# Performance work log

Measured on AMD Instinct MI355X. Metric: run time of the kernel, lower is better.

## Reference

```python
import jax, jax.numpy as jnp
import numpy as np


def setup_inputs() -> dict:
    key = jax.random.key(0)
    k1, k2, k3 = jax.random.split(key, 3)
    B, T, F, U = 32, 4096, 512, 512
    x = jax.random.normal(k1, (B, T, F), dtype=jnp.float32)
    W = jax.random.normal(k2, (F, U), dtype=jnp.float32)
    b = jnp.zeros((U,), dtype=jnp.float32)
    V = jax.random.uniform(k3, (U, 1), dtype=jnp.float32)
    return {"x": x, "W": W, "b": b, "V": V}


def reference(x, W, b, V):
    # u = tanh(x @ W + b): [B, T, U]
    u = jnp.tanh(jnp.einsum('btf,fu->btu', x, W) + b)
    # scores = u @ V: [B, T, 1]; softmax over time (dim=1)
    a = jax.nn.softmax(jnp.einsum('btu,uo->bto', u, V), axis=1)
    # weighted sum pooling over time -> [B, F]
    return jnp.sum(x * a, axis=1)
```

## Files before the change

### kernel.cpp

```cpp
#include <hip/hip_runtime.h>


#define XT 4096
#define XF 512
#define XU 512

typedef __attribute__((ext_vector_type(8))) short short8;
typedef __attribute__((ext_vector_type(16))) float f32x16;

__device__ inline void cvt_hilo(float x, unsigned short &h, unsigned short &l) {
  unsigned u = __builtin_bit_cast(unsigned, x);
  h = (unsigned short)(u >> 16);
  float hf = __builtin_bit_cast(float, u & 0xFFFF0000u);
  float lo = x - hf;
  l = (unsigned short)(__builtin_bit_cast(unsigned, lo) >> 16);
}

__device__ inline float tanh_fast(float z) {
  float e = __expf(2.0f * z);
  return 1.0f - 2.0f * __builtin_amdgcn_rcpf(e + 1.0f);
}

__global__ void wconv_kernel(const float *__restrict__ W,
                             unsigned short *__restrict__ whi,
                             unsigned short *__restrict__ wlo) {
  int t2 = blockIdx.x * 256 + threadIdx.x;
  int l = t2 & 31;
  int g = (t2 >> 5) & 1;
  int t = (t2 >> 6) & 15;
  int s = t2 >> 10;
  short8 hv, lv;
#pragma unroll
  for (int j = 0; j < 8; ++j) {
    unsigned short h, lo;
    cvt_hilo(W[(size_t)(s * 16 + g * 8 + j) * XU + t * 32 + l], h, lo);
    hv[j] = (short)h;
    lv[j] = (short)lo;
  }
  size_t off = (size_t)s * 8192 + t * 512 + g * 256 + l * 8;
  *(short8 *)(whi + off) = hv;
  *(short8 *)(wlo + off) = lv;
}

#define MFMA(a, b, c) __builtin_amdgcn_mfma_f32_32x32x16_bf16(a, b, c, 0, 0, 0)

__global__ __launch_bounds__(512, 2)
void gemm_scores_kernel(const float *__restrict__ x,
                        const unsigned short *__restrict__ whi,
                        const unsigned short *__restrict__ wlo,
                        const float *__restrict__ bias,
                        const float *__restrict__ V,
                        float *__restrict__ partial,
                        float *__restrict__ pstats) {
  __shared__ float scb[512];
  __shared__ float warr[128];
  __shared__ float red[1536];

  const int tid = threadIdx.x;
  const int lane = tid & 63;
  const int wave = tid >> 6;
  const int wr = wave >> 2;
  const int wc = wave & 3;
  const int l31 = lane & 31;
  const int half = lane >> 5;
  const size_t rowbase = (size_t)blockIdx.x * 128;

  f32x16 acc[2][4];
#pragma unroll
  for (int a = 0; a < 2; ++a)
#pragma unroll
    for (int c = 0; c < 4; ++c)
#pragma unroll
      for (int r = 0; r < 16; ++r) acc[a][c][r] = 0.f;

  const float *xr0 = x + (rowbase + wr * 64 + l31) * XF + half * 8;
  const float *xr1 = xr0 + 32 * XF;
  const unsigned short *whp = whi + (size_t)(wc * 4) * 512 + lane * 8;
  const unsigned short *wlp = wlo + (size_t)(wc * 4) * 512 + lane * 8;

#pragma unroll 1
  for (int s = 0; s < 32; ++s) {
    short8 bh[4], bl[4];
    const unsigned short *p = whp + (size_t)s * 8192;
    const unsigned short *q = wlp + (size_t)s * 8192;
#pragma unroll
    for (int cf = 0; cf < 4; ++cf) {
      bh[cf] = *(const short8 *)(p + cf * 512);
      bl[cf] = *(const short8 *)(q + cf * 512);
    }
    float4 a00 = *(const float4 *)(xr0 + s * 16);
    float4 a01 = *(const float4 *)(xr0 + s * 16 + 4);
    float4 a10 = *(const float4 *)(xr1 + s * 16);
    float4 a11 = *(const float4 *)(xr1 + s * 16 + 4);

    short8 ah0, al0, ah1, al1;
    {
      float v0[8] = {a00.x, a00.y, a00.z, a00.w, a01.x, a01.y, a01.z, a01.w};
      float v1[8] = {a10.x, a10.y, a10.z, a10.w, a11.x, a11.y, a11.z, a11.w};
#pragma unroll
      for (int j = 0; j < 8; ++j) {
        unsigned short h, lo;
        cvt_hilo(v0[j], h, lo);
        ah0[j] = (short)h; al0[j] = (short)lo;
        cvt_hilo(v1[j], h, lo);
        ah1[j] = (short)h; al1[j] = (short)lo;
      }
    }

#pragma unroll
    for (int cf = 0; cf < 4; ++cf) {
      acc[0][cf] = MFMA(ah0, bh[cf], acc[0][cf]);
      acc[1][cf] = MFMA(ah1, bh[cf], acc[1][cf]);
      acc[0][cf] = MFMA(al0, bh[cf], acc[0][cf]);
      acc[1][cf] = MFMA(al1, bh[cf], acc[1][cf]);
      acc[0][cf] = MFMA(ah0, bl[cf], acc[0][cf]);
      acc[1][cf] = MFMA(ah1, bl[cf], acc[1][cf]);
    }
  }

  float sc[2][16];
#pragma unroll
  for (int rf = 0; rf < 2; ++rf)
#pragma unroll
    for (int r = 0; r < 16; ++r) sc[rf][r] = 0.f;

#pragma unroll
  for (int cf = 0; cf < 4; ++cf) {
    int n = wc * 128 + cf * 32 + l31;
    float vv = V[n];
    float bb = bias[n];
#pragma unroll
    for (int rf = 0; rf < 2; ++rf)
#pragma unroll
      for (int r = 0; r < 16; ++r)
        sc[rf][r] += tanh_fast(acc[rf][cf][r] + bb) * vv;
  }
#pragma unroll
  for (int m = 1; m <= 16; m <<= 1) {
#pragma unroll
    for (int rf = 0; rf < 2; ++rf)
#pragma unroll
      for (int r = 0; r < 16; ++r)
        sc[rf][r] += __shfl_xor(sc[rf][r], m, 64);
  }
  if (l31 == 0) {
#pragma unroll
    for (int rf = 0; rf < 2; ++rf)
#pragma unroll
      for (int r = 0; r < 16; ++r) {
        int row = wr * 64 + rf * 32 + (r & 3) + 8 * (r >> 2) + 4 * half;
        scb[wc * 128 + row] = sc[rf][r];
      }
  }
  __syncthreads();

  __shared__ float sarr[128];
  if (tid < 128)
    sarr[tid] = scb[tid] + scb[128 + tid] + scb[256 + tid] + scb[384 + tid];
  __syncthreads();
  float mloc = -1e30f;
#pragma unroll 8
  for (int i = 0; i < 128; ++i) mloc = fmaxf(mloc, sarr[i]);
  if (tid < 128) warr[tid] = __expf(sarr[tid] - mloc);
  __syncthreads();

  const int rg = tid >> 7;
  const int c4 = tid & 127;
  const float *xp = x + rowbase * XF;
  float4 pa = {0.f, 0.f, 0.f, 0.f};
#pragma unroll 8
  for (int i = 0; i < 32; ++i) {
    int r = rg * 32 + i;
    float4 v = *(const float4 *)(xp + (size_t)r * XF + c4 * 4);
    float wv = warr[r];
    pa.x += wv * v.x;
    pa.y += wv * v.y;
    pa.z += wv * v.z;
    pa.w += wv * v.w;
  }
  if (rg > 0) {
    float *rp = red + (rg - 1) * 512 + c4 * 4;
    rp[0] = pa.x; rp[1] = pa.y; rp[2] = pa.z; rp[3] = pa.w;
  }
  __syncthreads();
  if (rg == 0) {
    const float *r0 = red + c4 * 4;
    float4 o;
    o.x = pa.x + r0[0] + r0[512] + r0[1024];
    o.y = pa.y + r0[1] + r0[513] + r0[1025];
    o.z = pa.z + r0[2] + r0[514] + r0[1026];
    o.w = pa.w + r0[3] + r0[515] + r0[1027];
    *(float4 *)(partial + (size_t)blockIdx.x * 512 + c4 * 4) = o;
  }
  if (tid == 0) {
    float l = 0.f;
#pragma unroll 8
    for (int i = 0; i < 128; ++i) l += warr[i];
    pstats[blockIdx.x * 2] = mloc;
    pstats[blockIdx.x * 2 + 1] = l;
  }
}

__global__ __launch_bounds__(512)
void combine_kernel(const float *__restrict__ partial,
                    const float *__restrict__ pstats,
                    float *__restrict__ out) {
  int b = blockIdx.x;
  int f = threadIdx.x;
  __shared__ float ml[32], ll[32];
  if (f < 32) {
    ml[f] = pstats[(b * 32 + f) * 2];
    ll[f] = pstats[(b * 32 + f) * 2 + 1];
  }
  __syncthreads();
  float M = -1e30f;
#pragma unroll
  for (int c = 0; c < 32; ++c) M = fmaxf(M, ml[c]);
  float L = 0.f;
#pragma unroll
  for (int c = 0; c < 32; ++c) L += __expf(ml[c] - M) * ll[c];
  float acc = 0.f;
#pragma unroll
  for (int c = 0; c < 32; ++c)
    acc += __expf(ml[c] - M) * partial[(size_t)(b * 32 + c) * 512 + f];
  out[b * XF + f] = acc / L;
}

extern "C" void kernel_launch(void *const *d_in, const int *in_sizes, int n_in,
                              void *d_out, int out_size, void *d_ws,
                              size_t ws_size, hipStream_t stream) {
  const float *x = (const float *)d_in[0];
  const float *W = (const float *)d_in[1];
  const float *bias = (const float *)d_in[2];
  const float *V = (const float *)d_in[3];
  float *out = (float *)d_out;

  unsigned short *whi = (unsigned short *)d_ws;
  unsigned short *wlo = whi + 262144;
  float *partial = (float *)((char *)d_ws + 1048576);
  float *pstats = (float *)((char *)d_ws + 1048576 + 2097152);

  wconv_kernel<<<128, 256, 0, stream>>>(W, whi, wlo);
  gemm_scores_kernel<<<1024, 512, 0, stream>>>(x, whi, wlo, bias, V, partial,
                                               pstats);
  combine_kernel<<<32, 512, 0, stream>>>(partial, pstats, out);
}
```

Measured before the change: 568.5 us.

## Shrink GEMM blocks to 32 rows with 4 waves and store partials as bf16

Each GEMM/score block now covers 32 time rows with 256 threads instead of 128 rows with 512 threads, giving 4096 blocks and higher occupancy per CU. The goal is better latency hiding and load balance. Each wave now loads its W fragments in two halves and keeps fewer accumulators. Per-block partial sums are rounded to bf16 to halve the extra partial traffic that the larger block count creates, and the combine kernel now merges 128 chunks per batch. The costs are W being reloaded by four times as many blocks and some precision lost in the partial sums.

```diff
diff --git a/kernel.cpp b/kernel.cpp
--- a/kernel.cpp
+++ b/kernel.cpp
@@ -4,16 +4,29 @@
 #define XT 4096
 #define XF 512
 #define XU 512
+#define NCHUNK 4096
+#define CPB 128
 
 typedef __attribute__((ext_vector_type(8))) short short8;
 typedef __attribute__((ext_vector_type(16))) float f32x16;
 
+__device__ inline unsigned fbits(float x) { return __builtin_bit_cast(unsigned, x); }
+
 __device__ inline void cvt_hilo(float x, unsigned short &h, unsigned short &l) {
-  unsigned u = __builtin_bit_cast(unsigned, x);
+  unsigned u = fbits(x);
   h = (unsigned short)(u >> 16);
   float hf = __builtin_bit_cast(float, u & 0xFFFF0000u);
   float lo = x - hf;
-  l = (unsigned short)(__builtin_bit_cast(unsigned, lo) >> 16);
+  l = (unsigned short)(fbits(lo) >> 16);
+}
+
+__device__ inline unsigned short bf16_rne(float v) {
+  unsigned u = fbits(v);
+  return (unsigned short)((u + 0x7FFFu + ((u >> 16) & 1u)) >> 16);
+}
+
+__device__ inline float bf16f(unsigned short h) {
+  return __builtin_bit_cast(float, (unsigned)h << 16);
 }
 
 __device__ inline float tanh_fast(float z) {
@@ -44,124 +57,99 @@
 
 #define MFMA(a, b, c) __builtin_amdgcn_mfma_f32_32x32x16_bf16(a, b, c, 0, 0, 0)
 
-__global__ __launch_bounds__(512, 2)
+__global__ __launch_bounds__(256, 4)
 void gemm_scores_kernel(const float *__restrict__ x,
                         const unsigned short *__restrict__ whi,
                         const unsigned short *__restrict__ wlo,
                         const float *__restrict__ bias,
                         const float *__restrict__ V,
-                        float *__restrict__ partial,
+                        unsigned short *__restrict__ partial,
                         float *__restrict__ pstats) {
-  __shared__ float scb[512];
-  __shared__ float warr[128];
-  __shared__ float red[1536];
+  __shared__ float scb[128];
+  __shared__ float sarr[32];
+  __shared__ float warr[32];
+  __shared__ float red[512];
 
   const int tid = threadIdx.x;
   const int lane = tid & 63;
-  const int wave = tid >> 6;
-  const int wr = wave >> 2;
-  const int wc = wave & 3;
+  const int wc = tid >> 6;
   const int l31 = lane & 31;
   const int half = lane >> 5;
-  const size_t rowbase = (size_t)blockIdx.x * 128;
-
-  f32x16 acc[2][4];
-#pragma unroll
-  for (int a = 0; a < 2; ++a)
-#pragma unroll
-    for (int c = 0; c < 4; ++c)
-#pragma unroll
-      for (int r = 0; r < 16; ++r) acc[a][c][r] = 0.f;
-
-  const float *xr0 = x + (rowbase + wr * 64 + l31) * XF + half * 8;
-  const float *xr1 = xr0 + 32 * XF;
+  const size_t rowbase = (size_t)blockIdx.x * 32;
+
+  f32x16 acc[4];
+#pragma unroll
+  for (int c = 0; c < 4; ++c)
+#pragma unroll
+    for (int r = 0; r < 16; ++r) acc[c][r] = 0.f;
+
+  const float *xr = x + (rowbase + l31) * XF + half * 8;
   const unsigned short *whp = whi + (size_t)(wc * 4) * 512 + lane * 8;
   const unsigned short *wlp = wlo + (size_t)(wc * 4) * 512 + lane * 8;
 
 #pragma unroll 1
   for (int s = 0; s < 32; ++s) {
-    short8 bh[4], bl[4];
-    const unsigned short *p = whp + (size_t)s * 8192;
-    const unsigned short *q = wlp + (size_t)s * 8192;
-#pragma unroll
-    for (int cf = 0; cf < 4; ++cf) {
-      bh[cf] = *(const short8 *)(p + cf * 512);
-      bl[cf] = *(const short8 *)(q + cf * 512);
-    }
-    float4 a00 = *(const float4 *)(xr0 + s * 16);
-    float4 a01 = *(const float4 *)(xr0 + s * 16 + 4);
-    float4 a10 = *(const float4 *)(xr1 + s * 16);
-    float4 a11 = *(const float4 *)(xr1 + s * 16 + 4);
-
-    short8 ah0, al0, ah1, al1;
+    float4 a0 = *(const float4 *)(xr + s * 16);
+    float4 a1 = *(const float4 *)(xr + s * 16 + 4);
+    short8 ah, al;
     {
-      float v0[8] = {a00.x, a00.y, a00.z, a00.w, a01.x, a01.y, a01.z, a01.w};
-      float v1[8] = {a10.x, a10.y, a10.z, a10.w, a11.x, a11.y, a11.z, a11.w};
+      float v[8] = {a0.x, a0.y, a0.z, a0.w, a1.x, a1.y, a1.z, a1.w};
 #pragma unroll
       for (int j = 0; j < 8; ++j) {
         unsigned short h, lo;
-        cvt_hilo(v0[j], h, lo);
-        ah0[j] = (short)h; al0[j] = (short)lo;
-        cvt_hilo(v1[j], h, lo);
-        ah1[j] = (short)h; al1[j] = (short)lo;
+        cvt_hilo(v[j], h, lo);
+        ah[j] = (short)h;
+        al[j] = (short)lo;
       }
     }
-
-#pragma unroll
-    for (int cf = 0; cf < 4; ++cf) {
-      acc[0][cf] = MFMA(ah0, bh[cf], acc[0][cf]);
-      acc[1][cf] = MFMA(ah1, bh[cf], acc[1][cf]);
-      acc[0][cf] = MFMA(al0, bh[cf], acc[0][cf]);
-      acc[1][cf] = MFMA(al1, bh[cf], acc[1][cf]);
-      acc[0][cf] = MFMA(ah0, bl[cf], acc[0][cf]);
-      acc[1][cf] = MFMA(ah1, bl[cf], acc[1][cf]);
+#pragma unroll
+    for (int p = 0; p < 2; ++p) {
+      const unsigned short *bp = whp + (size_t)s * 8192 + p * 1024;
+      const unsigned short *bq = wlp + (size_t)s * 8192 + p * 1024;
+      short8 bh0 = *(const short8 *)(bp);
+      short8 bh1 = *(const short8 *)(bp + 512);
+      short8 bl0 = *(const short8 *)(bq);
+      short8 bl1 = *(const short8 *)(bq + 512);
+      acc[2 * p] = MFMA(ah, bh0, acc[2 * p]);
+      acc[2 * p + 1] = MFMA(ah, bh1, acc[2 * p + 1]);
+      acc[2 * p] = MFMA(al, bh0, acc[2 * p]);
+      acc[2 * p + 1] = MFMA(al, bh1, acc[2 * p + 1]);
+      acc[2 * p] = MFMA(ah, bl0, acc[2 * p]);
+      acc[2 * p + 1] = MFMA(ah, bl1, acc[2 * p + 1]);
     }
   }
 
-  float sc[2][16];
-#pragma unroll
-  for (int rf = 0; rf < 2; ++rf)
-#pragma unroll
-    for (int r = 0; r < 16; ++r) sc[rf][r] = 0.f;
-
+  float sc[16];
+#pragma unroll
+  for (int r = 0; r < 16; ++r) sc[r] = 0.f;
 #pragma unroll
   for (int cf = 0; cf < 4; ++cf) {
     int n = wc * 128 + cf * 32 + l31;
     float vv = V[n];
     float bb = bias[n];
 #pragma unroll
-    for (int rf = 0; rf < 2; ++rf)
-#pragma unroll
-      for (int r = 0; r < 16; ++r)
-        sc[rf][r] += tanh_fast(acc[rf][cf][r] + bb) * vv;
-  }
-#pragma unroll
-  for (int m = 1; m <= 16; m <<= 1) {
-#pragma unroll
-    for (int rf = 0; rf < 2; ++rf)
-#pragma unroll
-      for (int r = 0; r < 16; ++r)
-        sc[rf][r] += __shfl_xor(sc[rf][r], m, 64);
-  }
+    for (int r = 0; r < 16; ++r) sc[r] += tanh_fast(acc[cf][r] + bb) * vv;
+  }
+#pragma unroll
+  for (int m = 1; m <= 16; m <<= 1)
+#pragma unroll
+    for (int r = 0; r < 16; ++r) sc[r] += __shfl_xor(sc[r], m, 64);
   if (l31 == 0) {
 #pragma unroll
-    for (int rf = 0; rf < 2; ++rf)
-#pragma unroll
-      for (int r = 0; r < 16; ++r) {
-        int row = wr * 64 + rf * 32 + (r & 3) + 8 * (r >> 2) + 4 * half;
-        scb[wc * 128 + row] = sc[rf][r];
-      }
-  }
-  __syncthreads();
-
-  __shared__ float sarr[128];
-  if (tid < 128)
-    sarr[tid] = scb[tid] + scb[128 + tid] + scb[256 + tid] + scb[384 + tid];
+    for (int r = 0; r < 16; ++r) {
+      int row = (r & 3) + 8 * (r >> 2) + 4 * half;
+      scb[wc * 32 + row] = sc[r];
+    }
+  }
+  __syncthreads();
+
+  if (tid < 32)
+    sarr[tid] = scb[tid] + scb[32 + tid] + scb[64 + tid] + scb[96 + tid];
   __syncthreads();
   float mloc = -1e30f;
 #pragma unroll 8
-  for (int i = 0; i < 128; ++i) mloc = fmaxf(mloc, sarr[i]);
-  if (tid < 128) warr[tid] = __expf(sarr[tid] - mloc);
+  for (int i = 0; i < 32; ++i) mloc = fmaxf(mloc, sarr[i]);
+  if (tid < 32) warr[tid] = __expf(sarr[tid] - mloc);
   __syncthreads();
 
   const int rg = tid >> 7;
@@ -169,8 +157,8 @@
   const float *xp = x + rowbase * XF;
   float4 pa = {0.f, 0.f, 0.f, 0.f};
 #pragma unroll 8
-  for (int i = 0; i < 32; ++i) {
-    int r = rg * 32 + i;
+  for (int i = 0; i < 16; ++i) {
+    int r = rg * 16 + i;
     float4 v = *(const float4 *)(xp + (size_t)r * XF + c4 * 4);
     float wv = warr[r];
     pa.x += wv * v.x;
@@ -178,51 +166,53 @@
     pa.z += wv * v.z;
     pa.w += wv * v.w;
   }
-  if (rg > 0) {
-    float *rp = red + (rg - 1) * 512 + c4 * 4;
+  if (rg == 1) {
+    float *rp = red + c4 * 4;
     rp[0] = pa.x; rp[1] = pa.y; rp[2] = pa.z; rp[3] = pa.w;
   }
   __syncthreads();
   if (rg == 0) {
     const float *r0 = red + c4 * 4;
-    float4 o;
-    o.x = pa.x + r0[0] + r0[512] + r0[1024];
-    o.y = pa.y + r0[1] + r0[513] + r0[1025];
-    o.z = pa.z + r0[2] + r0[514] + r0[1026];
-    o.w = pa.w + r0[3] + r0[515] + r0[1027];
-    *(float4 *)(partial + (size_t)blockIdx.x * 512 + c4 * 4) = o;
+    unsigned short o[4];
+    o[0] = bf16_rne(pa.x + r0[0]);
+    o[1] = bf16_rne(pa.y + r0[1]);
+    o[2] = bf16_rne(pa.z + r0[2]);
+    o[3] = bf16_rne(pa.w + r0[3]);
+    *(uint2 *)(partial + (size_t)blockIdx.x * 512 + c4 * 4) =
+        *(const uint2 *)o;
   }
   if (tid == 0) {
     float l = 0.f;
-#pragma unroll 8
-    for (int i = 0; i < 128; ++i) l += warr[i];
+#pragma unroll
+    for (int i = 0; i < 32; ++i) l += warr[i];
     pstats[blockIdx.x * 2] = mloc;
     pstats[blockIdx.x * 2 + 1] = l;
   }
 }
 
 __global__ __launch_bounds__(512)
-void combine_kernel(const float *__restrict__ partial,
+void combine_kernel(const unsigned short *__restrict__ partial,
                     const float *__restrict__ pstats,
                     float *__restrict__ out) {
   int b = blockIdx.x;
   int f = threadIdx.x;
-  __shared__ float ml[32], ll[32];
-  if (f < 32) {
-    ml[f] = pstats[(b * 32 + f) * 2];
-    ll[f] = pstats[(b * 32 + f) * 2 + 1];
+  __shared__ float ml[CPB], ll[CPB];
+  if (f < CPB) {
+    ml[f] = pstats[(b * CPB + f) * 2];
+    ll[f] = pstats[(b * CPB + f) * 2 + 1];
   }
   __syncthreads();
   float M = -1e30f;
-#pragma unroll
-  for (int c = 0; c < 32; ++c) M = fmaxf(M, ml[c]);
+#pragma unroll 8
+  for (int c = 0; c < CPB; ++c) M = fmaxf(M, ml[c]);
   float L = 0.f;
-#pragma unroll
-  for (int c = 0; c < 32; ++c) L += __expf(ml[c] - M) * ll[c];
   float acc = 0.f;
-#pragma unroll
-  for (int c = 0; c < 32; ++c)
-    acc += __expf(ml[c] - M) * partial[(size_t)(b * 32 + c) * 512 + f];
+#pragma unroll 4
+  for (int c = 0; c < CPB; ++c) {
+    float e = __expf(ml[c] - M);
+    L += e * ll[c];
+    acc += e * bf16f(partial[(size_t)(b * CPB + c) * 512 + f]);
+  }
   out[b * XF + f] = acc / L;
 }
 
@@ -237,11 +227,11 @@
 
   unsigned short *whi = (unsigned short *)d_ws;
   unsigned short *wlo = whi + 262144;
-  float *partial = (float *)((char *)d_ws + 1048576);
-  float *pstats = (float *)((char *)d_ws + 1048576 + 2097152);
+  unsigned short *partial = (unsigned short *)((char *)d_ws + 1048576);
+  float *pstats = (float *)((char *)d_ws + 1048576 + 4194304);
 
   wconv_kernel<<<128, 256, 0, stream>>>(W, whi, wlo);
-  gemm_scores_kernel<<<1024, 512, 0, stream>>>(x, whi, wlo, bias, V, partial,
-                                               pstats);
+  gemm_scores_kernel<<<NCHUNK, 256, 0, stream>>>(x, whi, wlo, bias, V, partial,
+                                                 pstats);
   combine_kernel<<<32, 512, 0, stream>>>(partial, pstats, out);
 }
```

Measured after the change: 627.0 us. 1.1x slower.

## Double-buffer W fragments in LDS via async loads and prefetch x

Applied to the files above, without the earlier changes.

The W hi/lo bf16 fragments are now staged cooperatively into a double-buffered LDS region with global_load_lds. The next k-slice is fetched while MFMAs run on the current one. The x row values for the next step are also prefetched into registers. This removes per-wave duplicated global loads of W and hides load latency behind the MFMA work. In exchange it adds a block-wide barrier every iteration and a 64KB LDS footprint that limits occupancy. The combine kernel's two exp loops are merged into one.

```diff
diff --git a/kernel.cpp b/kernel.cpp
--- a/kernel.cpp
+++ b/kernel.cpp
@@ -4,16 +4,25 @@
 #define XT 4096
 #define XF 512
 #define XU 512
+#define CPB 32
 
 typedef __attribute__((ext_vector_type(8))) short short8;
 typedef __attribute__((ext_vector_type(16))) float f32x16;
 
+__device__ inline unsigned fbits(float x) { return __builtin_bit_cast(unsigned, x); }
+
 __device__ inline void cvt_hilo(float x, unsigned short &h, unsigned short &l) {
-  unsigned u = __builtin_bit_cast(unsigned, x);
+  unsigned u = fbits(x);
   h = (unsigned short)(u >> 16);
   float hf = __builtin_bit_cast(float, u & 0xFFFF0000u);
   float lo = x - hf;
-  l = (unsigned short)(__builtin_bit_cast(unsigned, lo) >> 16);
+  l = (unsigned short)(fbits(lo) >> 16);
+}
+
+__device__ inline void async_ld16(const void *g, void *l) {
+  __builtin_amdgcn_global_load_lds(
+      (const __attribute__((address_space(1))) unsigned int *)g,
+      (__attribute__((address_space(3))) unsigned int *)l, 16, 0, 0);
 }
 
 __device__ inline float tanh_fast(float z) {
@@ -52,7 +61,9 @@
                         const float *__restrict__ V,
                         float *__restrict__ partial,
                         float *__restrict__ pstats) {
+  __shared__ unsigned short bsm[32768];
   __shared__ float scb[512];
+  __shared__ float sarr[128];
   __shared__ float warr[128];
   __shared__ float red[1536];
 
@@ -75,28 +86,52 @@
 
   const float *xr0 = x + (rowbase + wr * 64 + l31) * XF + half * 8;
   const float *xr1 = xr0 + 32 * XF;
-  const unsigned short *whp = whi + (size_t)(wc * 4) * 512 + lane * 8;
-  const unsigned short *wlp = wlo + (size_t)(wc * 4) * 512 + lane * 8;
+  const int bfrag = (wc * 4) * 512 + half * 256 + l31 * 8;
+
+  const int c0 = wave * 4;
+
+#pragma unroll
+  for (int i = 0; i < 4; ++i) {
+    int c = c0 + i;
+    const unsigned short *src =
+        (c < 16 ? whi + c * 512 : wlo + (c - 16) * 512) + lane * 8;
+    async_ld16(src, bsm + (c < 16 ? c * 512 : 8192 + (c - 16) * 512) + lane * 8);
+  }
+  float4 raw[2][4];
+  raw[0][0] = *(const float4 *)(xr0);
+  raw[0][1] = *(const float4 *)(xr0 + 4);
+  raw[0][2] = *(const float4 *)(xr1);
+  raw[0][3] = *(const float4 *)(xr1 + 4);
 
 #pragma unroll 1
   for (int s = 0; s < 32; ++s) {
-    short8 bh[4], bl[4];
-    const unsigned short *p = whp + (size_t)s * 8192;
-    const unsigned short *q = wlp + (size_t)s * 8192;
-#pragma unroll
-    for (int cf = 0; cf < 4; ++cf) {
-      bh[cf] = *(const short8 *)(p + cf * 512);
-      bl[cf] = *(const short8 *)(q + cf * 512);
+    const int cur = s & 1, nxt = cur ^ 1;
+    __syncthreads();
+
+    if (s < 31) {
+      const unsigned short *hsl = whi + (size_t)(s + 1) * 8192;
+      const unsigned short *lsl = wlo + (size_t)(s + 1) * 8192;
+#pragma unroll
+      for (int i = 0; i < 4; ++i) {
+        int c = c0 + i;
+        const unsigned short *src =
+            (c < 16 ? hsl + c * 512 : lsl + (c - 16) * 512) + lane * 8;
+        async_ld16(src, bsm + nxt * 16384 +
+                            (c < 16 ? c * 512 : 8192 + (c - 16) * 512) +
+                            lane * 8);
+      }
+      raw[nxt][0] = *(const float4 *)(xr0 + (s + 1) * 16);
+      raw[nxt][1] = *(const float4 *)(xr0 + (s + 1) * 16 + 4);
+      raw[nxt][2] = *(const float4 *)(xr1 + (s + 1) * 16);
+      raw[nxt][3] = *(const float4 *)(xr1 + (s + 1) * 16 + 4);
     }
-    float4 a00 = *(const float4 *)(xr0 + s * 16);
-    float4 a01 = *(const float4 *)(xr0 + s * 16 + 4);
-    float4 a10 = *(const float4 *)(xr1 + s * 16);
-    float4 a11 = *(const float4 *)(xr1 + s * 16 + 4);
 
     short8 ah0, al0, ah1, al1;
     {
-      float v0[8] = {a00.x, a00.y, a00.z, a00.w, a01.x, a01.y, a01.z, a01.w};
-      float v1[8] = {a10.x, a10.y, a10.z, a10.w, a11.x, a11.y, a11.z, a11.w};
+      float v0[8] = {raw[cur][0].x, raw[cur][0].y, raw[cur][0].z, raw[cur][0].w,
+                     raw[cur][1].x, raw[cur][1].y, raw[cur][1].z, raw[cur][1].w};
+      float v1[8] = {raw[cur][2].x, raw[cur][2].y, raw[cur][2].z, raw[cur][2].w,
+                     raw[cur][3].x, raw[cur][3].y, raw[cur][3].z, raw[cur][3].w};
 #pragma unroll
       for (int j = 0; j < 8; ++j) {
         unsigned short h, lo;
@@ -107,14 +142,17 @@
       }
     }
 
+    const unsigned short *bb = bsm + cur * 16384 + bfrag;
 #pragma unroll
     for (int cf = 0; cf < 4; ++cf) {
-      acc[0][cf] = MFMA(ah0, bh[cf], acc[0][cf]);
-      acc[1][cf] = MFMA(ah1, bh[cf], acc[1][cf]);
-      acc[0][cf] = MFMA(al0, bh[cf], acc[0][cf]);
-      acc[1][cf] = MFMA(al1, bh[cf], acc[1][cf]);
-      acc[0][cf] = MFMA(ah0, bl[cf], acc[0][cf]);
-      acc[1][cf] = MFMA(ah1, bl[cf], acc[1][cf]);
+      short8 bh = *(const short8 *)(bb + cf * 512);
+      short8 bl = *(const short8 *)(bb + cf * 512 + 8192);
+      acc[0][cf] = MFMA(ah0, bh, acc[0][cf]);
+      acc[1][cf] = MFMA(ah1, bh, acc[1][cf]);
+      acc[0][cf] = MFMA(al0, bh, acc[0][cf]);
+      acc[1][cf] = MFMA(al1, bh, acc[1][cf]);
+      acc[0][cf] = MFMA(ah0, bl, acc[0][cf]);
+      acc[1][cf] = MFMA(ah1, bl, acc[1][cf]);
     }
   }
 
@@ -128,12 +166,12 @@
   for (int cf = 0; cf < 4; ++cf) {
     int n = wc * 128 + cf * 32 + l31;
     float vv = V[n];
-    float bb = bias[n];
+    float bb2 = bias[n];
 #pragma unroll
     for (int rf = 0; rf < 2; ++rf)
 #pragma unroll
       for (int r = 0; r < 16; ++r)
-        sc[rf][r] += tanh_fast(acc[rf][cf][r] + bb) * vv;
+        sc[rf][r] += tanh_fast(acc[rf][cf][r] + bb2) * vv;
   }
 #pragma unroll
   for (int m = 1; m <= 16; m <<= 1) {
@@ -143,6 +181,7 @@
       for (int r = 0; r < 16; ++r)
         sc[rf][r] += __shfl_xor(sc[rf][r], m, 64);
   }
+  __syncthreads();
   if (l31 == 0) {
 #pragma unroll
     for (int rf = 0; rf < 2; ++rf)
@@ -154,7 +193,6 @@
   }
   __syncthreads();
 
-  __shared__ float sarr[128];
   if (tid < 128)
     sarr[tid] = scb[tid] + scb[128 + tid] + scb[256 + tid] + scb[384 + tid];
   __syncthreads();
@@ -207,22 +245,23 @@
                     float *__restrict__ out) {
   int b = blockIdx.x;
   int f = threadIdx.x;
-  __shared__ float ml[32], ll[32];
-  if (f < 32) {
-    ml[f] = pstats[(b * 32 + f) * 2];
-    ll[f] = pstats[(b * 32 + f) * 2 + 1];
+  __shared__ float ml[CPB], ll[CPB];
+  if (f < CPB) {
+    ml[f] = pstats[(b * CPB + f) * 2];
+    ll[f] = pstats[(b * CPB + f) * 2 + 1];
   }
   __syncthreads();
   float M = -1e30f;
 #pragma unroll
-  for (int c = 0; c < 32; ++c) M = fmaxf(M, ml[c]);
+  for (int c = 0; c < CPB; ++c) M = fmaxf(M, ml[c]);
   float L = 0.f;
-#pragma unroll
-  for (int c = 0; c < 32; ++c) L += __expf(ml[c] - M) * ll[c];
   float acc = 0.f;
 #pragma unroll
-  for (int c = 0; c < 32; ++c)
-    acc += __expf(ml[c] - M) * partial[(size_t)(b * 32 + c) * 512 + f];
+  for (int c = 0; c < CPB; ++c) {
+    float e = __expf(ml[c] - M);
+    L += e * ll[c];
+    acc += e * partial[(size_t)(b * CPB + c) * 512 + f];
+  }
   out[b * XF + f] = acc / L;
 }
 
```

After: 856.3 us. +50.6%, slower.
